# Kernel tuning notes

Hardware: AMD Instinct MI355X
Metric: run time of the kernel (lower is better)

Reference implementation:

```python
import jax, jax.numpy as jnp
import numpy as np

N_BIT = 4
GROUP = 128
ALPHA_W = 1.0   # group_size > -1 forces weight alpha to 1.0
ALPHA_A = 0.9   # searched input alpha
TOKENS, D_IN, D_OUT = 2048, 2048, 2048


def _int_grid(n_bit):
    B = n_bit - 1
    v = [0.0] + [float(s * i) for i in range(1, 2 ** B) for s in (1, -1)]
    v = np.sort(np.asarray(v, np.float32)) * (32.0 / 2 ** B)
    return v


def _outlier_grid(n_bit, exp_bit=2, exp_base=5):
    B = n_bit - 1
    mant_bit = B - exp_bit
    vals = []
    for i in range(exp_base, exp_base + 2 ** exp_bit):
        for j in range(2 ** mant_bit):
            if i == exp_base and j == 0:
                continue
            v = 2.0 ** i * (1.0 + 2.0 ** (-mant_bit) * j)
            vals += [v, -v]
    return np.sort(np.asarray(vals, np.float32))


_QG = _int_grid(N_BIT)
MAX_Q = float(_QG.max())              # 28.0 for 4-bit int grid
MERGED_GRID = jnp.asarray(np.concatenate([_QG, _outlier_grid(N_BIT)]))  # [29]


def get_quant(x, alpha, group_size):
    """Faithful jax port of get_quant(): per-group scale, nearest merged-grid
    quantization, roll-based outlier/victim masking, fp16 dequant."""
    org_shape = x.shape
    if group_size == -2:
        t = x.reshape(-1)
        mean, std = t.mean(), t.std(ddof=1)
    else:
        t = x.reshape(-1, group_size) if group_size > 0 else x
        mean = t.mean(axis=1, keepdims=True)
        std = t.std(axis=1, ddof=1, keepdims=True)
    normal_max = jnp.maximum(jnp.abs(mean + 3 * std), jnp.abs(mean - 3 * std))
    scales = normal_max * alpha / MAX_Q
    # nearest grid point over merged quant+outlier grid (the chunk loop in the
    # original is memory-chunking only; math is identical done whole)
    labels = jnp.argmin(jnp.abs((t / scales)[..., None] - MERGED_GRID), axis=-1)
    qf = MERGED_GRID[labels].reshape(-1)
    # victim masking: outliers (|q|>32) steal their paired neighbor's slot
    mask = jnp.abs(qf) > 32.0
    victim_odd = jnp.roll(mask, 1).at[::2].set(False)
    victim_even = jnp.roll(mask & ~victim_odd, -1).at[1::2].set(False)
    qf = jnp.where(victim_odd | victim_even, 0.0, qf)
    if group_size >= -1:
        qf = qf.reshape(t.shape)
    deq = (qf * scales).astype(jnp.float16)
    return deq.reshape(org_shape)


def setup_inputs() -> dict:
    key = jax.random.key(0)
    k1, k2 = jax.random.split(key)
    x = jax.random.normal(k1, (TOKENS, D_IN), dtype=jnp.float32)
    weight = jax.random.normal(k2, (D_OUT, D_IN), dtype=jnp.float32) * 0.02
    return {"x": x, "weight": weight}


def reference(x, weight):
    # runtime path of OliVe_Linear.forward (post-calibration), group_size=128
    w_deq = get_quant(weight, ALPHA_W, GROUP).astype(jnp.float32)
    x_deq = get_quant(x, ALPHA_A, GROUP).astype(jnp.float32)
    return x_deq @ w_deq.T  # [tokens, out_features]
```

## Files before the change

kernel.cpp:

```cpp
#include <hip/hip_runtime.h>
#include <hip/hip_fp16.h>
#include <stdint.h>

#define TOKENS 2048
#define DIM    2048
#define GROUP  128
#define NGK    16

typedef __attribute__((ext_vector_type(4)))  int   i32x4;
typedef __attribute__((ext_vector_type(4)))  float f32x4;


__device__ __forceinline__ float nearest_q4(float u) {
  float qi = fminf(fmaxf(rintf(u), -7.f), 7.f);
  float a = fabsf(u);
  float m = a <= 14.f ? 12.f : a <= 20.f ? 16.f : a <= 28.f ? 24.f
          : a <= 40.f ? 32.f : a <= 56.f ? 48.f : a <= 80.f ? 64.f : 96.f;
  float qo = copysignf(m, u);
  return (fabsf(u - qo) < fabsf(u - qi)) ? qo : qi;
}

__global__ __launch_bounds__(256) void quant2_kernel(
    const float* __restrict__ x, const float* __restrict__ w,
    int8_t* __restrict__ q8,
    float* __restrict__ ssxT,
    float* __restrict__ sswT) {
  const int wid  = threadIdx.x >> 6;
  const int lane = threadIdx.x & 63;
  const int l    = lane & 31;
  const int g    = blockIdx.x * 8 + wid * 2 + (lane >> 5);
  const int NG1  = TOKENS * DIM / GROUP;

  const float alpha = (g < NG1) ? 0.9f : 1.0f;
  const float* src  = (g < NG1) ? x : w;
  const int grow    = (g < NG1) ? g : g - NG1;
  const size_t sbase = (size_t)grow * GROUP + l * 4;

  const float4 v = *reinterpret_cast<const float4*>(src + sbase);

  float s  = (v.x + v.y) + (v.z + v.w);
  float ss = fmaf(v.x, v.x, fmaf(v.y, v.y, fmaf(v.z, v.z, v.w * v.w)));
#pragma unroll
  for (int off = 16; off > 0; off >>= 1) {
    s  += __shfl_xor(s,  off, 64);
    ss += __shfl_xor(ss, off, 64);
  }
  const float mean = s * (1.0f / 128.0f);
  const float var  = fmaf(-mean, s, ss) * (1.0f / 127.0f);
  const float scale = fmaf(3.0f, sqrtf(var), fabsf(mean)) * (alpha / 28.0f);
  const float rs4 = 0.25f / scale;

  const float u0 = v.x * rs4, u1 = v.y * rs4, u2 = v.z * rs4, u3 = v.w * rs4;
  const float amax = fmaxf(fmaxf(fabsf(u0), fabsf(u1)),
                           fmaxf(fabsf(u2), fabsf(u3)));

  int i0, i1, i2, i3;
  if (__any(amax >= 9.5f)) {
    float q0 = nearest_q4(u0);
    float q1 = nearest_q4(u1);
    float q2 = nearest_q4(u2);
    float q3 = nearest_q4(u3);
    if (fabsf(q0) > 8.0f)      q1 = 0.0f;
    else if (fabsf(q1) > 8.0f) q0 = 0.0f;
    if (fabsf(q2) > 8.0f)      q3 = 0.0f;
    else if (fabsf(q3) > 8.0f) q2 = 0.0f;
    i0 = (int)q0; i1 = (int)q1; i2 = (int)q2; i3 = (int)q3;
  } else {
    i0 = (int)fminf(fmaxf(rintf(u0), -7.f), 7.f);
    i1 = (int)fminf(fmaxf(rintf(u1), -7.f), 7.f);
    i2 = (int)fminf(fmaxf(rintf(u2), -7.f), 7.f);
    i3 = (int)fminf(fmaxf(rintf(u3), -7.f), 7.f);
  }

  const int p = (i0 & 255) | ((i1 & 255) << 8) |
                ((i2 & 255) << 16) | ((i3 & 255) << 24);
  reinterpret_cast<int*>(q8)[(size_t)g * 32 + l] = p;

  if (l == 0) {
    const float ssc = 4.0f * scale;
    if (g < NG1) ssxT[(grow & 15) * 2048 + (grow >> 4)] = ssc;
    else         sswT[(grow & 15) * 2048 + (grow >> 4)] = ssc;
  }
}


__device__ __forceinline__ void gload_lds16(const int8_t* g, char* l) {
  __builtin_amdgcn_global_load_lds(
      (__attribute__((address_space(1))) uint32_t*)g,
      (__attribute__((address_space(3))) uint32_t*)l, 16, 0, 0);
}

__global__ __launch_bounds__(256, 4) void gemm_kernel(
    const int8_t* __restrict__ Aq, const int8_t* __restrict__ Bq,
    const float* __restrict__ ssxT, const float* __restrict__ sswT,
    float* __restrict__ C) {
  __shared__ char lds_raw[2 * 16384 + 8192];
  float* ssx_l = (float*)(lds_raw + 32768);
  float* ssw_l = (float*)(lds_raw + 32768 + 4096);

  const int tid  = threadIdx.x;
  const int lane = tid & 63;
  const int wid  = tid >> 6;
  const int wr   = wid >> 1;
  const int wc   = wid & 1;
  const int r15  = lane & 15;
  const int hi4  = lane >> 4;

  const int bid = blockIdx.x;
  const int c   = bid & 7;
  const int idx = bid >> 3;
  const int bm  = ((c & 3) << 3) + (idx >> 4);
  const int bn  = ((c >> 2) << 4) + (idx & 15);

  const int8_t* gA = Aq + (size_t)(bm * 64) * DIM;
  const int8_t* gB = Bq + (size_t)(bn * 64) * DIM;

  auto stage = [&](char* buf, int g) {
#pragma unroll
    for (int i = 0; i < 2; ++i) {
      int P   = (i * 256 + tid) * 16;
      int row = P >> 7;
      int cb  = (P & 127) ^ ((row & 7) << 4);
      gload_lds16(gA + (size_t)row * DIM + g * 128 + cb, buf + P);
    }
#pragma unroll
    for (int i = 0; i < 2; ++i) {
      int P   = (i * 256 + tid) * 16;
      int row = P >> 7;
      int cb  = (P & 127) ^ ((row & 7) << 4);
      gload_lds16(gB + (size_t)row * DIM + g * 128 + cb, buf + 8192 + P);
    }
  };

  {
    int f = tid * 4;
    *reinterpret_cast<f32x4*>(&ssx_l[f]) =
        *reinterpret_cast<const f32x4*>(&ssxT[(f >> 6) * 2048 + bm * 64 + (f & 63)]);
  }
  {
    int f = tid * 4;
    *reinterpret_cast<f32x4*>(&ssw_l[f]) =
        *reinterpret_cast<const f32x4*>(&sswT[(f >> 6) * 2048 + bn * 64 + (f & 63)]);
  }
  __syncthreads();

  f32x4 accf[2][2] = {};
  const i32x4 zacc = {};

  auto compute = [&](const char* buf, int gk) {
    const char* cA = buf;
    const char* cB = buf + 8192;
    i32x4 acci[2][2];
#pragma unroll
    for (int kh = 0; kh < 2; ++kh) {
      const int kb = kh * 64 + hi4 * 16;
      i32x4 af[2], bf[2];
#pragma unroll
      for (int mt = 0; mt < 2; ++mt) {
        int row = wr * 32 + mt * 16 + r15;
        int pc  = kb ^ ((row & 7) << 4);
        af[mt] = *reinterpret_cast<const i32x4*>(cA + (row << 7) + pc);
      }
#pragma unroll
      for (int nt = 0; nt < 2; ++nt) {
        int row = wc * 32 + nt * 16 + r15;
        int pc  = kb ^ ((row & 7) << 4);
        bf[nt] = *reinterpret_cast<const i32x4*>(cB + (row << 7) + pc);
      }
      __builtin_amdgcn_s_setprio(1);
#pragma unroll
      for (int mt = 0; mt < 2; ++mt)
#pragma unroll
        for (int nt = 0; nt < 2; ++nt)
          acci[mt][nt] = __builtin_amdgcn_mfma_i32_16x16x64_i8(
              af[mt], bf[nt], kh == 0 ? zacc : acci[mt][nt], 0, 0, 0);
      __builtin_amdgcn_s_setprio(0);
    }
    float sw[2];
#pragma unroll
    for (int nt = 0; nt < 2; ++nt)
      sw[nt] = ssw_l[gk * 64 + wc * 32 + nt * 16 + r15];
#pragma unroll
    for (int mt = 0; mt < 2; ++mt) {
      f32x4 sx = *reinterpret_cast<const f32x4*>(
          &ssx_l[gk * 64 + wr * 32 + mt * 16 + 4 * hi4]);
#pragma unroll
      for (int nt = 0; nt < 2; ++nt)
#pragma unroll
        for (int e = 0; e < 4; ++e)
          accf[mt][nt][e] += sx[e] * (sw[nt] * (float)acci[mt][nt][e]);
    }
  };

  char* S0 = lds_raw;
  char* S1 = lds_raw + 16384;

  stage(S0, 0);
  for (int j = 0; j < NGK; ++j) {
    if (j + 1 < NGK) {
      stage((j & 1) ? S0 : S1, j + 1);
      asm volatile("s_waitcnt vmcnt(4)" ::: "memory");
    } else {
      asm volatile("s_waitcnt vmcnt(0)" ::: "memory");
    }
    __builtin_amdgcn_s_barrier();
    compute((j & 1) ? S1 : S0, j);
    __builtin_amdgcn_s_barrier();
  }

  const int crow0 = bm * 64 + wr * 32 + 4 * hi4;
  const int ccol0 = bn * 64 + wc * 32 + r15;
#pragma unroll
  for (int mt = 0; mt < 2; ++mt)
#pragma unroll
    for (int nt = 0; nt < 2; ++nt)
#pragma unroll
      for (int r = 0; r < 4; ++r) {
        int row = crow0 + mt * 16 + r;
        int col = ccol0 + nt * 16;
        C[(size_t)row * DIM + col] = accf[mt][nt][r];
      }
}


extern "C" void kernel_launch(void* const* d_in, const int* in_sizes, int n_in,
                              void* d_out, int out_size, void* d_ws,
                              size_t ws_size, hipStream_t stream) {
  const float* x = (const float*)d_in[0];
  const float* w = (const float*)d_in[1];
  float* out = (float*)d_out;

  int8_t* qx   = (int8_t*)d_ws;
  int8_t* qw   = qx + (size_t)TOKENS * DIM;
  float*  ssxT = (float*)(qw + (size_t)DIM * DIM);
  float*  sswT = ssxT + NGK * 2048;

  const int ngroups = 2 * TOKENS * DIM / GROUP;
  quant2_kernel<<<ngroups / 8, 256, 0, stream>>>(x, w, qx, ssxT, sswT);

  gemm_kernel<<<1024, 256, 0, stream>>>(qx, qw, ssxT, sswT, out);
}
```

Baseline: 31.53 us.

## Load GEMM B fragments directly from global into registers, bypassing LDS

The int8 weight (B) tile is no longer staged through LDS. Each wave now loads its B MFMA fragments straight from global memory into double-buffered registers, which halves the LDS footprint and removes the LDS reads of B. The main loop is unrolled by two to alternate between even and odd register buffers, and the vmcnt waits are adjusted to match. The trade-off is higher register pressure, and because waves with the same column index each fetch the same B data, global and L2 traffic for B is duplicated. The prologue also stages the second A buffer twice, which is redundant work.

```diff
diff --git a/kernel.cpp b/kernel.cpp
--- a/kernel.cpp
+++ b/kernel.cpp
@@ -94,9 +94,9 @@
     const int8_t* __restrict__ Aq, const int8_t* __restrict__ Bq,
     const float* __restrict__ ssxT, const float* __restrict__ sswT,
     float* __restrict__ C) {
-  __shared__ char lds_raw[2 * 16384 + 8192];
-  float* ssx_l = (float*)(lds_raw + 32768);
-  float* ssw_l = (float*)(lds_raw + 32768 + 4096);
+  __shared__ char lds_raw[2 * 8192 + 8192];
+  float* ssx_l = (float*)(lds_raw + 16384);
+  float* ssw_l = (float*)(lds_raw + 16384 + 4096);
 
   const int tid  = threadIdx.x;
   const int lane = tid & 63;
@@ -123,13 +123,16 @@
       int cb  = (P & 127) ^ ((row & 7) << 4);
       gload_lds16(gA + (size_t)row * DIM + g * 128 + cb, buf + P);
     }
-#pragma unroll
-    for (int i = 0; i < 2; ++i) {
-      int P   = (i * 256 + tid) * 16;
-      int row = P >> 7;
-      int cb  = (P & 127) ^ ((row & 7) << 4);
-      gload_lds16(gB + (size_t)row * DIM + g * 128 + cb, buf + 8192 + P);
-    }
+  };
+
+  auto loadB = [&](i32x4 (&bf)[2][2], int g) {
+#pragma unroll
+    for (int nt = 0; nt < 2; ++nt)
+#pragma unroll
+      for (int kh = 0; kh < 2; ++kh)
+        bf[nt][kh] = *reinterpret_cast<const i32x4*>(
+            gB + (size_t)(wc * 32 + nt * 16 + r15) * DIM +
+            g * 128 + kh * 64 + hi4 * 16);
   };
 
   {
@@ -142,38 +145,29 @@
     *reinterpret_cast<f32x4*>(&ssw_l[f]) =
         *reinterpret_cast<const f32x4*>(&sswT[(f >> 6) * 2048 + bn * 64 + (f & 63)]);
   }
-  __syncthreads();
 
   f32x4 accf[2][2] = {};
   const i32x4 zacc = {};
 
-  auto compute = [&](const char* buf, int gk) {
-    const char* cA = buf;
-    const char* cB = buf + 8192;
+  auto compute = [&](const char* cA, const i32x4 (&bf)[2][2], int gk) {
     i32x4 acci[2][2];
 #pragma unroll
     for (int kh = 0; kh < 2; ++kh) {
       const int kb = kh * 64 + hi4 * 16;
-      i32x4 af[2], bf[2];
+      i32x4 af[2];
 #pragma unroll
       for (int mt = 0; mt < 2; ++mt) {
         int row = wr * 32 + mt * 16 + r15;
         int pc  = kb ^ ((row & 7) << 4);
         af[mt] = *reinterpret_cast<const i32x4*>(cA + (row << 7) + pc);
       }
-#pragma unroll
-      for (int nt = 0; nt < 2; ++nt) {
-        int row = wc * 32 + nt * 16 + r15;
-        int pc  = kb ^ ((row & 7) << 4);
-        bf[nt] = *reinterpret_cast<const i32x4*>(cB + (row << 7) + pc);
-      }
       __builtin_amdgcn_s_setprio(1);
 #pragma unroll
       for (int mt = 0; mt < 2; ++mt)
 #pragma unroll
         for (int nt = 0; nt < 2; ++nt)
           acci[mt][nt] = __builtin_amdgcn_mfma_i32_16x16x64_i8(
-              af[mt], bf[nt], kh == 0 ? zacc : acci[mt][nt], 0, 0, 0);
+              af[mt], bf[nt][kh], kh == 0 ? zacc : acci[mt][nt], 0, 0, 0);
       __builtin_amdgcn_s_setprio(0);
     }
     float sw[2];
@@ -193,19 +187,40 @@
   };
 
   char* S0 = lds_raw;
-  char* S1 = lds_raw + 16384;
+  char* S1 = lds_raw + 8192;
+
+  i32x4 bf_e[2][2], bf_o[2][2];
 
   stage(S0, 0);
-  for (int j = 0; j < NGK; ++j) {
-    if (j + 1 < NGK) {
-      stage((j & 1) ? S0 : S1, j + 1);
-      asm volatile("s_waitcnt vmcnt(4)" ::: "memory");
-    } else {
-      asm volatile("s_waitcnt vmcnt(0)" ::: "memory");
-    }
-    __builtin_amdgcn_s_barrier();
-    compute((j & 1) ? S1 : S0, j);
-    __builtin_amdgcn_s_barrier();
+  stage(S1, 1);
+  loadB(bf_e, 0);
+  __syncthreads();
+
+  for (int t = 0; t < 16; t += 2) {
+    {
+      if (t + 1 < NGK) {
+        stage(S1, t + 1);
+        loadB(bf_o, t + 1);
+        asm volatile("s_waitcnt vmcnt(6)" ::: "memory");
+      } else {
+        asm volatile("s_waitcnt vmcnt(0)" ::: "memory");
+      }
+      __builtin_amdgcn_s_barrier();
+      compute(S0, bf_e, t);
+      __builtin_amdgcn_s_barrier();
+    }
+    {
+      if (t + 2 < NGK) {
+        stage(S0, t + 2);
+        loadB(bf_e, t + 2);
+        asm volatile("s_waitcnt vmcnt(6)" ::: "memory");
+      } else {
+        asm volatile("s_waitcnt vmcnt(0)" ::: "memory");
+      }
+      __builtin_amdgcn_s_barrier();
+      compute(S1, bf_o, t + 1);
+      __builtin_amdgcn_s_barrier();
+    }
   }
 
   const int crow0 = bm * 64 + wr * 32 + 4 * hi4;
```

Result: slower. 50.58 us (+60.4%).

## Fuse quantization and int8 GEMM into one cooperative persistent kernel

Applied to the files above, without the earlier changes.

Replaces the two separate launches (quantize, then GEMM) with one cooperative kernel of 512 blocks. Each block first quantizes 128 groups, then waits at a grid-wide sync, and then computes two GEMM output tiles in sequence. The aim is to remove the second launch and the gap between kernels. In exchange it adds a grid barrier, gives the GEMM only 512 blocks for 1024 tiles, and keeps a fallback to the two-kernel path if the cooperative launch fails.

```diff
diff --git a/kernel.cpp b/kernel.cpp
--- a/kernel.cpp
+++ b/kernel.cpp
@@ -1,6 +1,9 @@
 #include <hip/hip_runtime.h>
+#include <hip/hip_cooperative_groups.h>
 #include <hip/hip_fp16.h>
 #include <stdint.h>
+
+namespace cg = cooperative_groups;
 
 #define TOKENS 2048
 #define DIM    2048
@@ -9,7 +12,6 @@
 
 typedef __attribute__((ext_vector_type(4)))  int   i32x4;
 typedef __attribute__((ext_vector_type(4)))  float f32x4;
-
 
 __device__ __forceinline__ float nearest_q4(float u) {
   float qi = fminf(fmaxf(rintf(u), -7.f), 7.f);
@@ -20,17 +22,17 @@
   return (fabsf(u - qo) < fabsf(u - qi)) ? qo : qi;
 }
 
-__global__ __launch_bounds__(256) void quant2_kernel(
-    const float* __restrict__ x, const float* __restrict__ w,
-    int8_t* __restrict__ q8,
-    float* __restrict__ ssxT,
-    float* __restrict__ sswT) {
-  const int wid  = threadIdx.x >> 6;
-  const int lane = threadIdx.x & 63;
-  const int l    = lane & 31;
-  const int g    = blockIdx.x * 8 + wid * 2 + (lane >> 5);
-  const int NG1  = TOKENS * DIM / GROUP;
-
+__device__ __forceinline__ void gload_lds16(const int8_t* g, char* l) {
+  __builtin_amdgcn_global_load_lds(
+      (__attribute__((address_space(1))) uint32_t*)g,
+      (__attribute__((address_space(3))) uint32_t*)l, 16, 0, 0);
+}
+
+__device__ __forceinline__ void quant_group(
+    int g, const float* __restrict__ x, const float* __restrict__ w,
+    int8_t* __restrict__ q8, float* __restrict__ ssxT,
+    float* __restrict__ sswT, int l) {
+  const int NG1 = TOKENS * DIM / GROUP;
   const float alpha = (g < NG1) ? 0.9f : 1.0f;
   const float* src  = (g < NG1) ? x : w;
   const int grow    = (g < NG1) ? g : g - NG1;
@@ -84,21 +86,25 @@
 }
 
 
-__device__ __forceinline__ void gload_lds16(const int8_t* g, char* l) {
-  __builtin_amdgcn_global_load_lds(
-      (__attribute__((address_space(1))) uint32_t*)g,
-      (__attribute__((address_space(3))) uint32_t*)l, 16, 0, 0);
-}
-
-__global__ __launch_bounds__(256, 4) void gemm_kernel(
-    const int8_t* __restrict__ Aq, const int8_t* __restrict__ Bq,
+__global__ __launch_bounds__(256) void quant2_kernel(
+    const float* __restrict__ x, const float* __restrict__ w,
+    int8_t* __restrict__ q8, float* __restrict__ ssxT,
+    float* __restrict__ sswT) {
+  const int wid  = threadIdx.x >> 6;
+  const int lane = threadIdx.x & 63;
+  const int g    = blockIdx.x * 8 + wid * 2 + (lane >> 5);
+  quant_group(g, x, w, q8, ssxT, sswT, lane & 31);
+}
+
+template <typename LDS>
+__device__ __forceinline__ void gemm_tile(
+    int bid, const int8_t* __restrict__ Aq, const int8_t* __restrict__ Bq,
     const float* __restrict__ ssxT, const float* __restrict__ sswT,
-    float* __restrict__ C) {
-  __shared__ char lds_raw[2 * 16384 + 8192];
+    float* __restrict__ C, LDS* lds_raw_v, int tid) {
+  char* lds_raw = (char*)lds_raw_v;
   float* ssx_l = (float*)(lds_raw + 32768);
   float* ssw_l = (float*)(lds_raw + 32768 + 4096);
 
-  const int tid  = threadIdx.x;
   const int lane = tid & 63;
   const int wid  = tid >> 6;
   const int wr   = wid >> 1;
@@ -106,7 +112,6 @@
   const int r15  = lane & 15;
   const int hi4  = lane >> 4;
 
-  const int bid = blockIdx.x;
   const int c   = bid & 7;
   const int idx = bid >> 3;
   const int bm  = ((c & 3) << 3) + (idx >> 4);
@@ -142,7 +147,6 @@
     *reinterpret_cast<f32x4*>(&ssw_l[f]) =
         *reinterpret_cast<const f32x4*>(&sswT[(f >> 6) * 2048 + bn * 64 + (f & 63)]);
   }
-  __syncthreads();
 
   f32x4 accf[2][2] = {};
   const i32x4 zacc = {};
@@ -196,6 +200,7 @@
   char* S1 = lds_raw + 16384;
 
   stage(S0, 0);
+  __syncthreads();
   for (int j = 0; j < NGK; ++j) {
     if (j + 1 < NGK) {
       stage((j & 1) ? S0 : S1, j + 1);
@@ -222,6 +227,40 @@
       }
 }
 
+__global__ __launch_bounds__(256, 4) void gemm_kernel(
+    const int8_t* __restrict__ Aq, const int8_t* __restrict__ Bq,
+    const float* __restrict__ ssxT, const float* __restrict__ sswT,
+    float* __restrict__ C) {
+  __shared__ char lds_raw[2 * 16384 + 8192];
+  gemm_tile(blockIdx.x, Aq, Bq, ssxT, sswT, C, lds_raw, threadIdx.x);
+}
+
+
+__global__ __launch_bounds__(256, 4) void fused_kernel(
+    const float* __restrict__ x, const float* __restrict__ w,
+    int8_t* __restrict__ q8, float* __restrict__ ssxT,
+    float* __restrict__ sswT, float* __restrict__ C) {
+  __shared__ char lds_raw[2 * 16384 + 8192];
+
+  const int tid  = threadIdx.x;
+  const int lane = tid & 63;
+  const int wid  = tid >> 6;
+  const int l    = lane & 31;
+
+  for (int it = 0; it < 16; ++it) {
+    const int g = blockIdx.x * 128 + it * 8 + wid * 2 + (lane >> 5);
+    quant_group(g, x, w, q8, ssxT, sswT, l);
+  }
+
+  cg::this_grid().sync();
+
+  const int8_t* Aq = q8;
+  const int8_t* Bq = q8 + (size_t)TOKENS * DIM;
+  gemm_tile(blockIdx.x,       Aq, Bq, ssxT, sswT, C, lds_raw, tid);
+  __syncthreads();
+  gemm_tile(blockIdx.x + 512, Aq, Bq, ssxT, sswT, C, lds_raw, tid);
+}
+
 
 extern "C" void kernel_launch(void* const* d_in, const int* in_sizes, int n_in,
                               void* d_out, int out_size, void* d_ws,
@@ -231,12 +270,18 @@
   float* out = (float*)d_out;
 
   int8_t* qx   = (int8_t*)d_ws;
-  int8_t* qw   = qx + (size_t)TOKENS * DIM;
-  float*  ssxT = (float*)(qw + (size_t)DIM * DIM);
+  float*  ssxT = (float*)(qx + 2 * (size_t)TOKENS * DIM);
   float*  sswT = ssxT + NGK * 2048;
 
-  const int ngroups = 2 * TOKENS * DIM / GROUP;
-  quant2_kernel<<<ngroups / 8, 256, 0, stream>>>(x, w, qx, ssxT, sswT);
-
-  gemm_kernel<<<1024, 256, 0, stream>>>(qx, qw, ssxT, sswT, out);
-}
+  void* args[] = {(void*)&x, (void*)&w, (void*)&qx,
+                  (void*)&ssxT, (void*)&sswT, (void*)&out};
+  hipError_t e = hipLaunchCooperativeKernel(
+      (const void*)fused_kernel, dim3(512), dim3(256), args, 0, stream);
+  if (e != hipSuccess) {
+    (void)hipGetLastError();
+    const int ngroups = 2 * TOKENS * DIM / GROUP;
+    quant2_kernel<<<ngroups / 8, 256, 0, stream>>>(x, w, qx, ssxT, sswT);
+    gemm_kernel<<<1024, 256, 0, stream>>>(
+        qx, qx + (size_t)TOKENS * DIM, ssxT, sswT, out);
+  }
+}
```

New measurement: 93.17 us. 196% more time.
